# Kernel optimization log

Hardware: AMD Instinct MI355X
Metric: run time of the kernel (lower is better)

The kernel has to match this reference:

```python
import jax, jax.numpy as jnp
import numpy as np
import math

N, D, H, KV, DH, E, F_, CH = 2048, 1024, 16, 4, 64, 8, 2048, 64
VOCAB = 32000
EPS = 1e-6
THETA = 10000.0
DT = 0.1
BASE_SCALE = 10.0


def rmsnorm(x, w):
    var = jnp.mean(jnp.square(x), axis=-1, keepdims=True)
    return x * jax.lax.rsqrt(var + EPS) * w


def rope_tables(positions):
    inv_freq = THETA ** (-jnp.arange(0, DH, 2, dtype=jnp.float32) / DH)  # [DH/2]
    ang = positions.astype(jnp.float32)[:, None] * inv_freq              # [N, DH/2]
    return jnp.cos(ang), jnp.sin(ang)


def apply_rotary(x, cos, sin):
    # x: [N, heads, DH]; NeoX half-split rotation
    x1, x2 = jnp.split(x, 2, axis=-1)
    c, s = cos[:, None, :], sin[:, None, :]
    return jnp.concatenate([x1 * c - x2 * s, x2 * c + x1 * s], axis=-1)


def setup_inputs() -> dict:
    key = jax.random.key(0)
    ks = jax.random.split(key, 20)
    nrm = lambda k, shp, std: (jax.random.normal(k, shp) * std).astype(jnp.float32)
    inp = {
        'hidden': jax.random.normal(ks[0], (N, D), jnp.float32),
        'positions': jnp.arange(N, dtype=jnp.int32),
        'velocity': jax.random.normal(ks[1], (N, D), jnp.float32) * 0.1,
        'token_ids': jax.random.randint(ks[2], (N,), 0, VOCAB),
        'mu_prev': jax.random.normal(ks[3], (N, D), jnp.float32) * 0.1,
        'ln1_w': jnp.ones((D,), jnp.float32),
        'ln2_w': jnp.ones((D,), jnp.float32),
        'wq': nrm(ks[4], (D, H * DH), 0.02),
        'wk': nrm(ks[5], (D, KV * DH), 0.02),
        'wv': nrm(ks[6], (D, KV * DH), 0.02),
        'wo': nrm(ks[7], (H * DH, D), 0.02),
        'w_mu_q': nrm(ks[8], (D, H * DH), 0.01),
        'w_mu_k': nrm(ks[9], (D, KV * DH), 0.01),
        'w_mu_v': nrm(ks[10], (D, KV * DH), 0.01),
        'qnorm_w': jnp.ones((DH,), jnp.float32),
        'knorm_w': jnp.ones((DH,), jnp.float32),
        'dyn_mu': jnp.zeros((D,), jnp.float32),
        'dyn_mu_proj_w': nrm(ks[11], (D, D), 0.01),
        'ctrl_in_w': nrm(ks[12], (2 * D, CH), 0.02),
        'ctrl_in_b': jnp.zeros((CH,), jnp.float32),
        'ctrl_out_w': nrm(ks[13], (CH, 3 * D), 0.01),
        'ctrl_out_b': jnp.concatenate([jnp.full((D,), 2.2), jnp.full((D,), -2.2), jnp.zeros((D,))]).astype(jnp.float32),
        'mu_router_w': nrm(ks[14], (D, E), 0.01),
        'w_gate': nrm(ks[15], (E, D, F_), 0.02),
        'w_up': nrm(ks[16], (E, D, F_), 0.02),
        'w_down': nrm(ks[17], (E, F_, D), 0.02),
    }
    return inp


def reference(hidden, positions, velocity, token_ids, mu_prev,
              ln1_w, ln2_w, wq, wk, wv, wo, w_mu_q, w_mu_k, w_mu_v,
              qnorm_w, knorm_w, dyn_mu, dyn_mu_proj_w,
              ctrl_in_w, ctrl_in_b, ctrl_out_w, ctrl_out_b,
              mu_router_w, w_gate, w_up, w_down):
    residual = hidden
    h = rmsnorm(hidden, ln1_w)
    # --- mu-guided GQA attention ---
    q = (h @ wq + mu_prev @ w_mu_q).reshape(N, H, DH)
    k = (h @ wk + mu_prev @ w_mu_k).reshape(N, KV, DH)
    v = (h @ wv + mu_prev @ w_mu_v).reshape(N, KV, DH)
    q = rmsnorm(q, qnorm_w)
    k = rmsnorm(k, knorm_w)
    cos, sin = rope_tables(positions)
    q = apply_rotary(q, cos, sin)
    k = apply_rotary(k, cos, sin)
    groups = H // KV
    k = jnp.repeat(k, groups, axis=1)  # [N, H, DH]
    v = jnp.repeat(v, groups, axis=1)
    scale = 1.0 / math.sqrt(DH)
    scores = jnp.einsum('nhd,mhd->hnm', q, k) * scale
    attn = jax.nn.softmax(scores, axis=-1)
    o = jnp.einsum('hnm,mhd->nhd', attn, v).reshape(N, H * DH) @ wo
    # --- INL dynamics (PID) ---
    hv = jnp.concatenate([o, velocity], axis=-1)
    ctrl = jax.nn.silu(hv @ ctrl_in_w + ctrl_in_b)
    co = ctrl @ ctrl_out_w + ctrl_out_b
    alpha_raw, beta_raw, gate_raw = co[:, :D], co[:, D:2 * D], co[:, 2 * D:]
    alpha = jax.nn.sigmoid(alpha_raw)
    beta = jnp.minimum(jax.nn.softplus(beta_raw), 2.0)
    gate = jax.nn.sigmoid(gate_raw)
    mu_cur = dyn_mu + o @ dyn_mu_proj_w
    err = o - mu_cur
    v_next = jnp.clip(alpha * velocity - beta * err, -10.0, 10.0)
    h_next = o + DT * gate * v_next
    hidden = residual + h_next
    # --- mu-guided token-routed MoE MLP ---
    residual2 = hidden
    x = rmsnorm(hidden, ln2_w)
    base_ids = (token_ids % E).astype(jnp.int32)
    mu_logits = mu_cur @ mu_router_w                        # [N, E]
    combined = jax.nn.one_hot(base_ids, E) * BASE_SCALE + mu_logits
    expert_ids = jnp.argmax(combined, axis=-1)              # [N]
    g = jnp.einsum('nd,edf->enf', x, w_gate)                # [E, N, F]
    u = jnp.einsum('nd,edf->enf', x, w_up)
    mid = jax.nn.silu(g) * u
    y_all = jnp.einsum('enf,efd->end', mid, w_down)         # [E, N, D]
    sel = jax.nn.one_hot(expert_ids, E)                     # [N, E]
    y = jnp.einsum('ne,end->nd', sel, y_all)
    hidden = residual2 + y
    return (hidden, v_next, mu_cur)
```

## Files before the change

### kernel.cpp

```cpp
#include <hip/hip_runtime.h>
#include <hip/hip_bf16.h>
#include <math.h>

typedef __hip_bfloat16 bf16;
typedef __attribute__((ext_vector_type(8))) short short8;
typedef __attribute__((ext_vector_type(4))) float floatx4;

#define N_TOK 2048
#define DM    1024
#define NH    16
#define NKV   4
#define DH    64
#define NE    8
#define FF    2048
#define CH    64

__device__ __forceinline__ float b2f(bf16 x) { return __bfloat162float(x); }
__device__ __forceinline__ bf16  f2b(float x) { return __float2bfloat16(x); }
__device__ __forceinline__ short f2s(float x) { bf16 t = __float2bfloat16(x); return *(short*)&t; }

#define GLL16(g, l) __builtin_amdgcn_global_load_lds( \
    (const __attribute__((address_space(1))) void*)(g), \
    (__attribute__((address_space(3))) void*)(l), 16, 0, 0)

__device__ __forceinline__ float blockReduceSum256(float v) {
    __shared__ float tmp[4];
    #pragma unroll
    for (int m = 1; m < 64; m <<= 1) v += __shfl_xor(v, m, 64);
    if ((threadIdx.x & 63) == 0) tmp[threadIdx.x >> 6] = v;
    __syncthreads();
    float r = tmp[0] + tmp[1] + tmp[2] + tmp[3];
    __syncthreads();
    return r;
}

__global__ __launch_bounds__(256) void k_transpose(
    const float* __restrict__ src, long sstrideE, int sN,
    bf16* __restrict__ dst, long dstrideE, int ldk)
{
    __shared__ float tile[64][65];
    const float* s = src + (long)blockIdx.z * sstrideE;
    bf16* d = dst + (long)blockIdx.z * dstrideE;
    int n0 = blockIdx.x * 64, k0 = blockIdx.y * 64;
    int tid = threadIdx.x;
    int c = tid & 63, r4 = tid >> 6;
    #pragma unroll
    for (int i = 0; i < 16; i++) {
        int r = i * 4 + r4;
        tile[r][c] = s[(long)(k0 + r) * sN + n0 + c];
    }
    __syncthreads();
    int c2 = (tid & 31) * 2, rr = tid >> 5;
    #pragma unroll
    for (int i = 0; i < 8; i++) {
        int r = i * 8 + rr;
        short2 o;
        o.x = f2s(tile[c2][r]);
        o.y = f2s(tile[c2 + 1][r]);
        *(short2*)(d + (long)(n0 + r) * ldk + k0 + c2) = o;
    }
}

__global__ __launch_bounds__(256) void k_prep(
    const float* __restrict__ hidden, const float* __restrict__ ln1_w,
    const float* __restrict__ mu_prev, const float* __restrict__ velocity,
    bf16* __restrict__ catA, bf16* __restrict__ ctrlA)
{
    int n = blockIdx.x, tid = threadIdx.x;
    float ss = 0.f, vals[4];
    #pragma unroll
    for (int i = 0; i < 4; i++) {
        int c = tid + i * 256;
        vals[i] = hidden[(long)n * DM + c];
        ss += vals[i] * vals[i];
        catA[(long)n * 2048 + 1024 + c] = f2b(mu_prev[(long)n * DM + c]);
        ctrlA[(long)n * 2048 + 1024 + c] = f2b(velocity[(long)n * DM + c]);
    }
    float tot = blockReduceSum256(ss);
    float r = rsqrtf(tot / (float)DM + 1e-6f);
    #pragma unroll
    for (int i = 0; i < 4; i++) {
        int c = tid + i * 256;
        catA[(long)n * 2048 + c] = f2b(vals[i] * r * ln1_w[c]);
    }
}

#define GEMM_WRITE  1
#define GEMM_BIAS   2
#define GEMM_WRITEB 4
#define GEMM_DOWN   8

__global__ __launch_bounds__(256) void k_gemm(
    const bf16* __restrict__ A, int lda,
    const bf16* __restrict__ Bt, int ldb, long strideBe,
    float* __restrict__ C, int ldc,
    const float* __restrict__ bias,
    bf16* __restrict__ Cb, int ldcb,
    int K, int flags,
    int nsplit, long strideKc,
    const int* __restrict__ grp_off,
    const int* __restrict__ perm,
    float* __restrict__ outp)
{
    __shared__ __align__(16) short As[128 * 32];
    __shared__ __align__(16) short Bs[128 * 32];
    int tid = threadIdx.x;
    int e = blockIdx.z, kc = 0;
    if (nsplit > 1) { e = blockIdx.z / nsplit; kc = blockIdx.z % nsplit; }
    int rowBase, rowsValid;
    const bf16* Bp = Bt;
    if (grp_off) {
        int r0 = grp_off[e], r1 = grp_off[e + 1];
        int rt = blockIdx.y * 128;
        rowsValid = (r1 - r0) - rt;
        if (rowsValid <= 0) return;
        if (rowsValid > 128) rowsValid = 128;
        rowBase = r0 + rt;
        Bp = Bt + (long)e * strideBe;
    } else {
        rowBase = blockIdx.y * 128;
        rowsValid = 128;
    }
    int n0 = blockIdx.x * 128;
    int Kc = K / nsplit;
    int kbeg = kc * Kc, kend = kbeg + Kc;

    floatx4 acc[4][4];
    #pragma unroll
    for (int i = 0; i < 4; i++)
        #pragma unroll
        for (int j = 0; j < 4; j++) acc[i][j] = (floatx4){0.f, 0.f, 0.f, 0.f};

    int wave = tid >> 6, lane = tid & 63;
    int wm = (wave >> 1) * 64, wn = (wave & 1) * 64;
    int lrow = lane & 15, quad = lane >> 4;

    int c0 = wave * 2;
    int srow0 = c0 * 16 + (lane >> 2);
    int srow1 = (c0 + 1) * 16 + (lane >> 2);
    int skoff = (lane & 3) * 8;
    short* ldsA0 = As + c0 * 512;
    short* ldsA1 = As + (c0 + 1) * 512;
    short* ldsB0 = Bs + c0 * 512;
    short* ldsB1 = Bs + (c0 + 1) * 512;

    for (int k0 = kbeg; k0 < kend; k0 += 32) {
        if (srow0 < rowsValid) GLL16(A + (long)(rowBase + srow0) * lda + k0 + skoff, ldsA0);
        if (srow1 < rowsValid) GLL16(A + (long)(rowBase + srow1) * lda + k0 + skoff, ldsA1);
        GLL16(Bp + (long)(n0 + srow0) * ldb + k0 + skoff, ldsB0);
        GLL16(Bp + (long)(n0 + srow1) * ldb + k0 + skoff, ldsB1);
        __syncthreads();
        short8 af[4], bfr[4];
        #pragma unroll
        for (int mi = 0; mi < 4; mi++)
            af[mi] = *(const short8*)(&As[(wm + mi * 16 + lrow) * 32 + quad * 8]);
        #pragma unroll
        for (int ni = 0; ni < 4; ni++)
            bfr[ni] = *(const short8*)(&Bs[(wn + ni * 16 + lrow) * 32 + quad * 8]);
        #pragma unroll
        for (int mi = 0; mi < 4; mi++)
            #pragma unroll
            for (int ni = 0; ni < 4; ni++)
                acc[mi][ni] = __builtin_amdgcn_mfma_f32_16x16x32_bf16(
                    af[mi], bfr[ni], acc[mi][ni], 0, 0, 0);
        __syncthreads();
    }

    #pragma unroll
    for (int mi = 0; mi < 4; mi++) {
        #pragma unroll
        for (int ni = 0; ni < 4; ni++) {
            #pragma unroll
            for (int r = 0; r < 4; r++) {
                int rl = wm + mi * 16 + quad * 4 + r;
                if (rl >= rowsValid) continue;
                int grow = rowBase + rl;
                int gcol = n0 + wn + ni * 16 + lrow;
                float v = acc[mi][ni][r];
                if (nsplit > 1) {
                    C[kc * strideKc + (long)grow * ldc + gcol] = v;
                    continue;
                }
                if (flags & GEMM_BIAS) v += bias[gcol];
                if (flags & GEMM_DOWN) {
                    int tok = perm[grow];
                    float* o = &outp[(long)tok * ldc + gcol];
                    *o = *o + v;
                } else {
                    if (flags & GEMM_WRITE) C[(long)grow * ldc + gcol] = v;
                    if (flags & GEMM_WRITEB) Cb[(long)grow * ldcb + gcol] = f2b(v);
                }
            }
        }
    }
}

__global__ __launch_bounds__(256) void k_red_wo(const float* __restrict__ p,
                                                float* __restrict__ o_f,
                                                bf16* __restrict__ ctrlA) {
    int n = blockIdx.x, tid = threadIdx.x;
    #pragma unroll
    for (int i = 0; i < 4; i++) {
        int c = tid + i * 256;
        float v = p[(long)n * DM + c] + p[(long)N_TOK * DM + (long)n * DM + c];
        o_f[(long)n * DM + c] = v;
        ctrlA[(long)n * 2048 + c] = f2b(v);
    }
}

__global__ __launch_bounds__(256) void k_red_down(const float* __restrict__ p,
                                                  const int* __restrict__ perm,
                                                  float* __restrict__ out0) {
    int r = blockIdx.x, tid = threadIdx.x;
    int tok = perm[r];
    #pragma unroll
    for (int i = 0; i < 4; i++) {
        int c = tid + i * 256;
        long idx = (long)r * DM + c;
        float v = p[idx] + p[(long)N_TOK * DM + idx] +
                  p[(long)2 * N_TOK * DM + idx] + p[(long)3 * N_TOK * DM + idx];
        out0[(long)tok * DM + c] += v;
    }
}

__global__ __launch_bounds__(256) void k_ctrl_gemm(
    const bf16* __restrict__ A,
    const bf16* __restrict__ Bt,
    float* __restrict__ part)
{
    __shared__ __align__(16) short As[128 * 32];
    __shared__ __align__(16) short Bs[64 * 32];
    int tid = threadIdx.x;
    int rowBase = blockIdx.x * 128;
    int kbeg = blockIdx.y * 256;
    int wave = tid >> 6, lane = tid & 63;
    int wm = wave * 32, lrow = lane & 15, quad = lane >> 4;
    int srow = lane >> 2, skoff = (lane & 3) * 8;

    floatx4 acc[2][4];
    #pragma unroll
    for (int i = 0; i < 2; i++)
        #pragma unroll
        for (int j = 0; j < 4; j++) acc[i][j] = (floatx4){0.f, 0.f, 0.f, 0.f};

    short* ldsA0 = As + (wave * 2) * 512;
    short* ldsA1 = As + (wave * 2 + 1) * 512;
    short* ldsB  = Bs + wave * 512;

    for (int k0 = kbeg; k0 < kbeg + 256; k0 += 32) {
        GLL16(A + (long)(rowBase + wave * 32 + srow) * 2048 + k0 + skoff, ldsA0);
        GLL16(A + (long)(rowBase + wave * 32 + 16 + srow) * 2048 + k0 + skoff, ldsA1);
        GLL16(Bt + (long)(wave * 16 + srow) * 2048 + k0 + skoff, ldsB);
        __syncthreads();
        short8 af[2], bfr[4];
        af[0] = *(const short8*)(&As[(wm + lrow) * 32 + quad * 8]);
        af[1] = *(const short8*)(&As[(wm + 16 + lrow) * 32 + quad * 8]);
        #pragma unroll
        for (int ni = 0; ni < 4; ni++)
            bfr[ni] = *(const short8*)(&Bs[(ni * 16 + lrow) * 32 + quad * 8]);
        #pragma unroll
        for (int mi = 0; mi < 2; mi++)
            #pragma unroll
            for (int ni = 0; ni < 4; ni++)
                acc[mi][ni] = __builtin_amdgcn_mfma_f32_16x16x32_bf16(
                    af[mi], bfr[ni], acc[mi][ni], 0, 0, 0);
        __syncthreads();
    }
    #pragma unroll
    for (int mi = 0; mi < 2; mi++)
        #pragma unroll
        for (int ni = 0; ni < 4; ni++)
            #pragma unroll
            for (int r = 0; r < 4; r++) {
                int grow = rowBase + wm + mi * 16 + quad * 4 + r;
                part[((long)blockIdx.y * N_TOK + grow) * 64 + ni * 16 + lrow] = acc[mi][ni][r];
            }
}

__global__ __launch_bounds__(256) void k_silu_ctrl(const float* __restrict__ part,
                                                   const float* __restrict__ b,
                                                   bf16* __restrict__ out) {
    int i = blockIdx.x * 256 + threadIdx.x;
    float a = b[i & 63];
    #pragma unroll
    for (int kc = 0; kc < 8; kc++) a += part[(long)kc * (N_TOK * 64) + i];
    out[i] = f2b(a / (1.f + __expf(-a)));
}

__global__ __launch_bounds__(256) void k_qkv_post(
    const float* __restrict__ qkvp, const int* __restrict__ positions,
    const float* __restrict__ qnw, const float* __restrict__ knw,
    bf16* __restrict__ q, bf16* __restrict__ k, bf16* __restrict__ v)
{
    int n = blockIdx.x;
    int wave = threadIdx.x >> 6, lane = threadIdx.x & 63;
    float pos = (float)positions[n];
    int i = lane & 31;
    float invf = exp2f(-(float)(2 * i) * (13.287712379549449f / 64.f));
    float ang = pos * invf;
    float c = cosf(ang), s = sinf(ang);

    #pragma unroll
    for (int si = 0; si < 6; si++) {
        int slot = wave + si * 4;
        long base = (long)n * 1536 +
                    (slot < 16 ? slot * 64
                               : (slot < 20 ? 1024 + (slot - 16) * 64
                                            : 1280 + (slot - 20) * 64));
        float val = qkvp[base + lane] + qkvp[(long)N_TOK * 1536 + base + lane];
        if (slot < 20) {
            float ss = val * val;
            #pragma unroll
            for (int m = 1; m < 64; m <<= 1) ss += __shfl_xor(ss, m, 64);
            float r = rsqrtf(ss / 64.f + 1e-6f);
            float wn = (slot < 16 ? qnw[lane] : knw[lane]);
            float xn = val * r * wn;
            float partner = __shfl_xor(xn, 32, 64);
            float out = (lane < 32) ? (xn * c - partner * s) : (xn * c + partner * s);
            if (slot < 16) q[((long)n * NH + slot) * 64 + lane] = f2b(out);
            else           k[((long)n * NKV + (slot - 16)) * 64 + lane] = f2b(out);
        } else {
            v[((long)n * NKV + (slot - 20)) * 64 + lane] = f2b(val);
        }
    }
}

__global__ __launch_bounds__(256) void k_vt(const bf16* __restrict__ v,
                                            bf16* __restrict__ vt) {
    __shared__ short tile[64][65];
    int kv = blockIdx.z, n0 = blockIdx.x * 64;
    int tid = threadIdx.x;
    int c = tid & 63, r4 = tid >> 6;
    const short* vs = (const short*)v;
    #pragma unroll
    for (int i = 0; i < 16; i++) {
        int r = i * 4 + r4;
        tile[r][c] = vs[(long)(n0 + r) * 256 + kv * 64 + c];
    }
    __syncthreads();
    #pragma unroll
    for (int i = 0; i < 16; i++) {
        int d = i * 4 + r4;
        ((short*)vt)[(long)(kv * 64 + d) * 2048 + n0 + c] = tile[c][d];
    }
}

__global__ __launch_bounds__(256) void k_attn(
    const bf16* __restrict__ q, const bf16* __restrict__ k,
    const bf16* __restrict__ vt,
    float* __restrict__ opart, float2* __restrict__ ml)
{
    const int h = blockIdx.y;
    const int qbase = blockIdx.x * 64;
    const int z = blockIdx.z;
    const int kvh = h >> 2;
    __shared__ __align__(16) short Qs[64 * 72];
    __shared__ __align__(16) short Ks[64 * 72];
    __shared__ __align__(16) short Vt[64 * 72];
    __shared__ __align__(16) short Ps[4 * 16 * 72];
    int tid = threadIdx.x, wave = tid >> 6, lane = tid & 63;
    int lrow = lane & 15, quad = lane >> 4;

    #pragma unroll
    for (int i = 0; i < 2; i++) {
        int lin = tid + i * 256;
        int r = lin >> 3, dc = (lin & 7) << 3;
        short8 vq = *(const short8*)(q + ((long)(qbase + r) * NH + h) * 64 + dc);
        *(short8*)&Qs[r * 72 + dc] = vq;
    }
    float m_i[4], l_i[4];
    floatx4 oacc[4];
    #pragma unroll
    for (int r = 0; r < 4; r++) { m_i[r] = -1e30f; l_i[r] = 0.f; }
    #pragma unroll
    for (int di = 0; di < 4; di++) oacc[di] = (floatx4){0.f, 0.f, 0.f, 0.f};
    const float scale = 0.125f;
    __syncthreads();

    const int kt0 = z * (N_TOK / 2);
    for (int kt = kt0; kt < kt0 + N_TOK / 2; kt += 64) {
        #pragma unroll
        for (int i = 0; i < 2; i++) {
            int lin = tid + i * 256;
            int r = lin >> 3, dc = (lin & 7) << 3;
            short8 k8 = *(const short8*)(k + ((long)(kt + r) * NKV + kvh) * 64 + dc);
            *(short8*)&Ks[r * 72 + dc] = k8;
            short8 v8 = *(const short8*)(vt + (long)(kvh * 64 + r) * 2048 + kt + dc);
            *(short8*)&Vt[r * 72 + dc] = v8;
        }
        __syncthreads();

        short8 aq0 = *(const short8*)&Qs[(wave * 16 + lrow) * 72 + quad * 8];
        short8 aq1 = *(const short8*)&Qs[(wave * 16 + lrow) * 72 + 32 + quad * 8];
        floatx4 sv[4];
        #pragma unroll
        for (int kn = 0; kn < 4; kn++) {
            short8 b0 = *(const short8*)&Ks[(kn * 16 + lrow) * 72 + quad * 8];
            short8 b1 = *(const short8*)&Ks[(kn * 16 + lrow) * 72 + 32 + quad * 8];
            floatx4 t = (floatx4){0.f, 0.f, 0.f, 0.f};
            t = __builtin_amdgcn_mfma_f32_16x16x32_bf16(aq0, b0, t, 0, 0, 0);
            t = __builtin_amdgcn_mfma_f32_16x16x32_bf16(aq1, b1, t, 0, 0, 0);
            sv[kn] = t;
        }
        #pragma unroll
        for (int kn = 0; kn < 4; kn++)
            #pragma unroll
            for (int r = 0; r < 4; r++) sv[kn][r] *= scale;

        #pragma unroll
        for (int r = 0; r < 4; r++) {
            float mx = fmaxf(fmaxf(sv[0][r], sv[1][r]), fmaxf(sv[2][r], sv[3][r]));
            #pragma unroll
            for (int msk = 1; msk < 16; msk <<= 1) mx = fmaxf(mx, __shfl_xor(mx, msk, 64));
            float mnew = fmaxf(m_i[r], mx);
            float alpha = __expf(m_i[r] - mnew);
            m_i[r] = mnew;
            l_i[r] *= alpha;
            #pragma unroll
            for (int di = 0; di < 4; di++) oacc[di][r] *= alpha;
            float rowsum = 0.f;
            #pragma unroll
            for (int kn = 0; kn < 4; kn++) {
                float pp = __expf(sv[kn][r] - mnew);
                sv[kn][r] = pp;
                rowsum += pp;
            }
            #pragma unroll
            for (int msk = 1; msk < 16; msk <<= 1) rowsum += __shfl_xor(rowsum, msk, 64);
            l_i[r] += rowsum;
        }
        #pragma unroll
        for (int kn = 0; kn < 4; kn++)
            #pragma unroll
            for (int r = 0; r < 4; r++)
                Ps[(wave * 16 + quad * 4 + r) * 72 + kn * 16 + lrow] = f2s(sv[kn][r]);
        __syncthreads();

        short8 ap0 = *(const short8*)&Ps[(wave * 16 + lrow) * 72 + quad * 8];
        short8 ap1 = *(const short8*)&Ps[(wave * 16 + lrow) * 72 + 32 + quad * 8];
        #pragma unroll
        for (int di = 0; di < 4; di++) {
            short8 bv0 = *(const short8*)&Vt[(di * 16 + lrow) * 72 + quad * 8];
            short8 bv1 = *(const short8*)&Vt[(di * 16 + lrow) * 72 + 32 + quad * 8];
            oacc[di] = __builtin_amdgcn_mfma_f32_16x16x32_bf16(ap0, bv0, oacc[di], 0, 0, 0);
            oacc[di] = __builtin_amdgcn_mfma_f32_16x16x32_bf16(ap1, bv1, oacc[di], 0, 0, 0);
        }
        __syncthreads();
    }

    #pragma unroll
    for (int di = 0; di < 4; di++)
        #pragma unroll
        for (int r = 0; r < 4; r++) {
            int n = qbase + wave * 16 + quad * 4 + r;
            opart[((long)z * N_TOK + n) * DM + h * 64 + di * 16 + lrow] = oacc[di][r];
        }
    if (lrow == 0) {
        #pragma unroll
        for (int r = 0; r < 4; r++) {
            int n = qbase + wave * 16 + quad * 4 + r;
            ml[(long)(z * NH + h) * N_TOK + n] = make_float2(m_i[r], l_i[r]);
        }
    }
}

__global__ __launch_bounds__(256) void k_attn_merge(
    const float* __restrict__ opart, const float2* __restrict__ ml,
    bf16* __restrict__ attn_out)
{
    int n = blockIdx.x, tid = threadIdx.x;
    __shared__ float2 sml[2][NH];
    if (tid < 32) {
        int z = tid >> 4, hh = tid & 15;
        sml[z][hh] = ml[(long)(z * NH + hh) * N_TOK + n];
    }
    __syncthreads();
    #pragma unroll
    for (int i = 0; i < 4; i++) {
        int c = tid + i * 256;
        int h = c >> 6;
        float2 a = sml[0][h], b = sml[1][h];
        float M = fmaxf(a.x, b.x);
        float w0 = __expf(a.x - M), w1 = __expf(b.x - M);
        float num = w0 * opart[(long)n * DM + c] +
                    w1 * opart[((long)N_TOK + n) * DM + c];
        float den = w0 * a.y + w1 * b.y;
        attn_out[(long)n * DM + c] = f2b(num / den);
    }
}

__global__ __launch_bounds__(256) void k_ode(
    const float* __restrict__ co, const float* __restrict__ o_f,
    const float* __restrict__ velocity, const float* __restrict__ mup,
    const float* __restrict__ dyn_mu, const float* __restrict__ hidden_in,
    const float* __restrict__ mu_router_w, const int* __restrict__ token_ids,
    const float* __restrict__ ln2_w,
    float* __restrict__ out0, float* __restrict__ out_vnext,
    float* __restrict__ out_mu, bf16* __restrict__ x_bf,
    int* __restrict__ expert_id, int* __restrict__ counts)
{
    int n = blockIdx.x, tid = threadIdx.x;
    __shared__ float mu_s[DM];
    __shared__ float red2[32][8];

    #pragma unroll
    for (int i = 0; i < 4; i++) {
        int c = tid + i * 256;
        mu_s[c] = mup[(long)n * DM + c] + mup[(long)N_TOK * DM + (long)n * DM + c]
                + dyn_mu[c];
    }
    __syncthreads();

    {
        int e = tid & 7, kc = tid >> 3;
        float a = 0.f;
        #pragma unroll
        for (int kk = 0; kk < 32; kk++) {
            int k = kc * 32 + kk;
            a += mu_s[k] * mu_router_w[k * NE + e];
        }
        red2[kc][e] = a;
    }
    __syncthreads();
    if (tid == 0) {
        int bid = token_ids[n] & (NE - 1);
        float best = -1e30f; int bi = 0;
        for (int e = 0; e < NE; e++) {
            float lg = (e == bid ? 10.f : 0.f);
            for (int j = 0; j < 32; j++) lg += red2[j][e];
            if (lg > best) { best = lg; bi = e; }
        }
        expert_id[n] = bi;
        atomicAdd(&counts[bi], 1);
    }

    float ssq = 0.f;
    float h1v[4];
    #pragma unroll
    for (int i = 0; i < 4; i++) {
        int c = tid + i * 256;
        float coa = co[(long)n * 3072 + c];
        float cob = co[(long)n * 3072 + DM + c];
        float cog = co[(long)n * 3072 + 2 * DM + c];
        float alpha = 1.f / (1.f + __expf(-coa));
        float sp = (cob > 20.f) ? cob : log1pf(__expf(cob));
        float beta = fminf(sp, 2.0f);
        float gate = 1.f / (1.f + __expf(-cog));
        float ov = o_f[(long)n * DM + c];
        float vv = velocity[(long)n * DM + c];
        float err = ov - mu_s[c];
        float vn = fminf(fmaxf(alpha * vv - beta * err, -10.f), 10.f);
        float hn = ov + 0.1f * gate * vn;
        float h1 = hidden_in[(long)n * DM + c] + hn;
        h1v[i] = h1;
        ssq += h1 * h1;
        out_vnext[(long)n * DM + c] = vn;
        out_mu[(long)n * DM + c] = mu_s[c];
        out0[(long)n * DM + c] = h1;
    }
    float tot = blockReduceSum256(ssq);
    float rstd = rsqrtf(tot / (float)DM + 1e-6f);
    #pragma unroll
    for (int i = 0; i < 4; i++) {
        int c = tid + i * 256;
        x_bf[(long)n * DM + c] = f2b(h1v[i] * rstd * ln2_w[c]);
    }
}

__global__ void k_zero8(int* counts, int* fill) {
    if (threadIdx.x < NE) { counts[threadIdx.x] = 0; fill[threadIdx.x] = 0; }
}
__global__ void k_offsets(const int* counts, int* off) {
    if (threadIdx.x == 0) {
        int a = 0;
        for (int e = 0; e < NE; e++) { off[e] = a; a += counts[e]; }
        off[NE] = a;
    }
}
__global__ void k_scatter(const int* expert_id, const int* off, int* fill, int* perm) {
    int n = blockIdx.x * 256 + threadIdx.x;
    if (n < N_TOK) {
        int e = expert_id[n];
        int p = off[e] + atomicAdd(&fill[e], 1);
        perm[p] = n;
    }
}
__global__ __launch_bounds__(256) void k_gather(const int* __restrict__ perm,
                                                const bf16* __restrict__ x,
                                                bf16* __restrict__ xg) {
    int r = blockIdx.x;
    int tok = perm[r];
    ((int2*)(xg + (long)r * DM))[threadIdx.x] =
        ((const int2*)(x + (long)tok * DM))[threadIdx.x];
}
__global__ __launch_bounds__(256) void k_silumul(const bf16* __restrict__ gu,
                                                 bf16* __restrict__ mid) {
    long i = (long)blockIdx.x * 256 + threadIdx.x;
    long r = i >> 11, c = i & 2047;
    float g = b2f(gu[r * 4096 + c]);
    float u = b2f(gu[r * 4096 + 2048 + c]);
    mid[i] = f2b(g / (1.f + __expf(-g)) * u);
}

extern "C" void kernel_launch(void* const* d_in, const int* in_sizes, int n_in,
                              void* d_out, int out_size, void* d_ws, size_t ws_size,
                              hipStream_t stream) {
    (void)in_sizes; (void)n_in; (void)out_size; (void)ws_size;
    const float* hidden     = (const float*)d_in[0];
    const int*   positions  = (const int*)d_in[1];
    const float* velocity   = (const float*)d_in[2];
    const int*   token_ids  = (const int*)d_in[3];
    const float* mu_prev    = (const float*)d_in[4];
    const float* ln1_w      = (const float*)d_in[5];
    const float* ln2_w      = (const float*)d_in[6];
    const float* wq         = (const float*)d_in[7];
    const float* wk         = (const float*)d_in[8];
    const float* wv         = (const float*)d_in[9];
    const float* wo         = (const float*)d_in[10];
    const float* w_mu_q     = (const float*)d_in[11];
    const float* w_mu_k     = (const float*)d_in[12];
    const float* w_mu_v     = (const float*)d_in[13];
    const float* qnorm_w    = (const float*)d_in[14];
    const float* knorm_w    = (const float*)d_in[15];
    const float* dyn_mu     = (const float*)d_in[16];
    const float* dyn_proj   = (const float*)d_in[17];
    const float* ctrl_in_w  = (const float*)d_in[18];
    const float* ctrl_in_b  = (const float*)d_in[19];
    const float* ctrl_out_w = (const float*)d_in[20];
    const float* ctrl_out_b = (const float*)d_in[21];
    const float* mu_router  = (const float*)d_in[22];
    const float* w_gate     = (const float*)d_in[23];
    const float* w_up       = (const float*)d_in[24];
    const float* w_down     = (const float*)d_in[25];

    float* out0 = (float*)d_out;
    float* out1 = out0 + (long)N_TOK * DM;
    float* out2 = out1 + (long)N_TOK * DM;

    char* p = (char*)d_ws;
    auto alloc = [&](size_t bytes) -> void* {
        void* r = (void*)p;
        p += (bytes + 255) & ~(size_t)255;
        return r;
    };
    bf16* WqkvT   = (bf16*)alloc((long)1536 * 2048 * 2);
    bf16* woT     = (bf16*)alloc((long)1024 * 1024 * 2);
    bf16* dynT    = (bf16*)alloc((long)1024 * 1024 * 2);
    bf16* ctrlinT = (bf16*)alloc((long)64 * 2048 * 2);
    bf16* ctrloutT= (bf16*)alloc((long)3072 * 64 * 2);
    bf16* gupT    = (bf16*)alloc((long)NE * 4096 * 1024 * 2);
    bf16* downT   = (bf16*)alloc((long)NE * 1024 * 2048 * 2);
    bf16*  catA   = (bf16*)alloc((long)N_TOK * 2048 * 2);
    bf16*  ctrlA  = (bf16*)alloc((long)N_TOK * 2048 * 2);
    float* xbuf   = (float*)alloc((long)N_TOK * 1536 * 4);
    bf16*  q_bf   = (bf16*)alloc((long)N_TOK * NH * DH * 2);
    bf16*  k_bf   = (bf16*)alloc((long)N_TOK * NKV * DH * 2);
    bf16*  v_bf   = (bf16*)alloc((long)N_TOK * NKV * DH * 2);
    bf16*  vt_bf  = (bf16*)alloc((long)NKV * DH * N_TOK * 2);
    float* o_f    = (float*)alloc((long)N_TOK * DM * 4);
    float* coGu   = (float*)alloc((long)N_TOK * 3072 * 4);
    float* splitb = (float*)alloc((long)4 * N_TOK * DM * 4);
    bf16*  ctrlbf = (bf16*)alloc((long)N_TOK * CH * 2);
    int*   expert_id = (int*)alloc(N_TOK * 4);
    int*   perm      = (int*)alloc(N_TOK * 4);
    int*   counts    = (int*)alloc(64 * 4);
    int*   fill      = (int*)alloc(64 * 4);
    int*   offs      = (int*)alloc(64 * 4);

    bf16*  attn_bf = catA;
    bf16*  x_bf    = (bf16*)xbuf;
    bf16*  xg_bf   = (bf16*)xbuf + (long)N_TOK * DM;
    float* cpart   = (float*)((bf16*)xbuf + (long)2 * N_TOK * DM);
    float* opart   = coGu;
    float2* ml     = (float2*)(coGu + (long)2 * N_TOK * DM);
    float* co_f    = coGu;
    bf16*  gu_bf   = (bf16*)coGu;
    bf16*  mid_bf  = (bf16*)o_f;

    dim3 blk(256);
    k_zero8<<<1, 64, 0, stream>>>(counts, fill);

    k_transpose<<<dim3(16,16,1), blk, 0, stream>>>(wq, 0, 1024, WqkvT, 0, 2048);
    k_transpose<<<dim3(4,16,1),  blk, 0, stream>>>(wk, 0, 256,  WqkvT + (long)1024*2048, 0, 2048);
    k_transpose<<<dim3(4,16,1),  blk, 0, stream>>>(wv, 0, 256,  WqkvT + (long)1280*2048, 0, 2048);
    k_transpose<<<dim3(16,16,1), blk, 0, stream>>>(w_mu_q, 0, 1024, WqkvT + 1024, 0, 2048);
    k_transpose<<<dim3(4,16,1),  blk, 0, stream>>>(w_mu_k, 0, 256,  WqkvT + (long)1024*2048 + 1024, 0, 2048);
    k_transpose<<<dim3(4,16,1),  blk, 0, stream>>>(w_mu_v, 0, 256,  WqkvT + (long)1280*2048 + 1024, 0, 2048);
    k_transpose<<<dim3(16,16,1), blk, 0, stream>>>(wo, 0, 1024, woT, 0, 1024);
    k_transpose<<<dim3(16,16,1), blk, 0, stream>>>(dyn_proj, 0, 1024, dynT, 0, 1024);
    k_transpose<<<dim3(1,32,1),  blk, 0, stream>>>(ctrl_in_w, 0, 64, ctrlinT, 0, 2048);
    k_transpose<<<dim3(48,1,1),  blk, 0, stream>>>(ctrl_out_w, 0, 3072, ctrloutT, 0, 64);
    k_transpose<<<dim3(32,16,NE), blk, 0, stream>>>(w_gate, (long)1024*2048, 2048,
        gupT, (long)4096*1024, 1024);
    k_transpose<<<dim3(32,16,NE), blk, 0, stream>>>(w_up, (long)1024*2048, 2048,
        gupT + (long)2048*1024, (long)4096*1024, 1024);
    k_transpose<<<dim3(16,32,NE), blk, 0, stream>>>(w_down, (long)2048*1024, 1024,
        downT, (long)1024*2048, 2048);

    k_prep<<<N_TOK, blk, 0, stream>>>(hidden, ln1_w, mu_prev, velocity, catA, ctrlA);

    k_gemm<<<dim3(12,16,2), blk, 0, stream>>>(catA, 2048, WqkvT, 2048, 0,
        splitb, 1536, nullptr, nullptr, 0, 2048, 0, 2, (long)N_TOK * 1536,
        nullptr, nullptr, nullptr);

    k_qkv_post<<<N_TOK, blk, 0, stream>>>(splitb, positions, qnorm_w, knorm_w, q_bf, k_bf, v_bf);
    k_vt<<<dim3(32,1,NKV), blk, 0, stream>>>(v_bf, vt_bf);
    k_attn<<<dim3(32,16,2), blk, 0, stream>>>(q_bf, k_bf, vt_bf, opart, ml);
    k_attn_merge<<<N_TOK, blk, 0, stream>>>(opart, ml, attn_bf);

    k_gemm<<<dim3(8,16,2), blk, 0, stream>>>(attn_bf, 1024, woT, 1024, 0,
        splitb, 1024, nullptr, nullptr, 0, 1024, 0, 2, (long)N_TOK * DM,
        nullptr, nullptr, nullptr);
    k_red_wo<<<N_TOK, blk, 0, stream>>>(splitb, o_f, ctrlA);

    k_gemm<<<dim3(8,16,2), blk, 0, stream>>>(ctrlA, 2048, dynT, 1024, 0,
        splitb, 1024, nullptr, nullptr, 0, 1024, 0, 2, (long)N_TOK * DM,
        nullptr, nullptr, nullptr);

    k_ctrl_gemm<<<dim3(16,8,1), blk, 0, stream>>>(ctrlA, ctrlinT, cpart);
    k_silu_ctrl<<<(N_TOK * CH) / 256, blk, 0, stream>>>(cpart, ctrl_in_b, ctrlbf);
    k_gemm<<<dim3(24,16,1), blk, 0, stream>>>(ctrlbf, 64, ctrloutT, 64, 0,
        co_f, 3072, ctrl_out_b, nullptr, 0, 64, GEMM_WRITE | GEMM_BIAS, 1, 0,
        nullptr, nullptr, nullptr);

    k_ode<<<N_TOK, blk, 0, stream>>>(co_f, o_f, velocity, splitb, dyn_mu, hidden,
        mu_router, token_ids, ln2_w, out0, out1, out2, x_bf, expert_id, counts);

    k_offsets<<<1, 64, 0, stream>>>(counts, offs);
    k_scatter<<<NE, blk, 0, stream>>>(expert_id, offs, fill, perm);
    k_gather<<<N_TOK, blk, 0, stream>>>(perm, x_bf, xg_bf);

    k_gemm<<<dim3(32,16,NE), blk, 0, stream>>>(xg_bf, 1024, gupT, 1024, (long)4096*1024,
        nullptr, 0, nullptr, gu_bf, 4096, 1024, GEMM_WRITEB, 1, 0,
        offs, nullptr, nullptr);
    k_silumul<<<(N_TOK * FF) / 256, blk, 0, stream>>>(gu_bf, mid_bf);
    k_gemm<<<dim3(8,16,NE*4), blk, 0, stream>>>(mid_bf, 2048, downT, 2048, (long)1024*2048,
        splitb, 1024, nullptr, nullptr, 0, 2048, 0, 4, (long)N_TOK * DM,
        offs, nullptr, nullptr);
    k_red_down<<<N_TOK, blk, 0, stream>>>(splitb, perm, out0);
}
```

Before: 648.0 us.

## Batch weight transposes, fuse MoE routing kernels, and rework attention with 4-way split

All thirteen weight transposes, plus the counter zeroing, now run as one table-driven launch with vectorized loads and stores. The offsets, scatter and gather kernels become one kernel that computes prefix offsets inline, and the grouped GEMM derives its row offsets from the counts. Attention moves to a 4-way KV split with a swizzled LDS layout and register-prefetched K/V tiles. It also folds the softmax scale and log2e into Q so exp2 can be used, skips the rescale when the running max grows by less than a threshold, and computes row sums with an MFMA against a ones vector. Buffers are reassigned to fit the larger partial outputs. This cuts launch overhead, LDS bank conflicts and attention latency, at the cost of more merge work and some bf16 precision in the row sums.

```diff
diff --git a/kernel.cpp b/kernel.cpp
--- a/kernel.cpp
+++ b/kernel.cpp
@@ -14,10 +14,13 @@
 #define NE    8
 #define FF    2048
 #define CH    64
+#define QSCL  0.18033688011112042f
 
 __device__ __forceinline__ float b2f(bf16 x) { return __bfloat162float(x); }
 __device__ __forceinline__ bf16  f2b(float x) { return __float2bfloat16(x); }
 __device__ __forceinline__ short f2s(float x) { bf16 t = __float2bfloat16(x); return *(short*)&t; }
+
+#define MFMA16(a, b, c) __builtin_amdgcn_mfma_f32_16x16x32_bf16(a, b, c, 0, 0, 0)
 
 #define GLL16(g, l) __builtin_amdgcn_global_load_lds( \
     (const __attribute__((address_space(1))) void*)(g), \
@@ -34,30 +37,51 @@
     return r;
 }
 
-__global__ __launch_bounds__(256) void k_transpose(
-    const float* __restrict__ src, long sstrideE, int sN,
-    bf16* __restrict__ dst, long dstrideE, int ldk)
-{
-    __shared__ float tile[64][65];
-    const float* s = src + (long)blockIdx.z * sstrideE;
-    bf16* d = dst + (long)blockIdx.z * dstrideE;
-    int n0 = blockIdx.x * 64, k0 = blockIdx.y * 64;
+struct TEnt {
+    const float* src; bf16* dst;
+    long sstride, dstride;
+    int sN, ldk, tN, tilesPer, start;
+};
+struct TTab { TEnt t[13]; };
+
+__global__ __launch_bounds__(256) void k_transpose_all(TTab tab, int* counts, int* fill) {
+    if (blockIdx.x == 0 && threadIdx.x < NE) {
+        counts[threadIdx.x] = 0;
+        fill[threadIdx.x] = 0;
+    }
+    int b = blockIdx.x;
+    int wi = 0;
+    #pragma unroll
+    for (int i = 1; i < 13; i++) if (b >= tab.t[i].start) wi = i;
+    const TEnt& w = tab.t[wi];
+    int local = b - w.start;
+    int e = local / w.tilesPer; local -= e * w.tilesPer;
+    int kt = local / w.tN, nt = local - kt * w.tN;
+    const float* s = w.src + (long)e * w.sstride;
+    bf16* d = w.dst + (long)e * w.dstride;
+    int n0 = nt * 64, k0 = kt * 64;
+
+    __shared__ float t[64][65];
     int tid = threadIdx.x;
-    int c = tid & 63, r4 = tid >> 6;
-    #pragma unroll
-    for (int i = 0; i < 16; i++) {
-        int r = i * 4 + r4;
-        tile[r][c] = s[(long)(k0 + r) * sN + n0 + c];
+    int c4 = (tid & 15) * 4, r0 = tid >> 4;
+    #pragma unroll
+    for (int i = 0; i < 4; i++) {
+        int row = r0 + i * 16;
+        float4 v = *(const float4*)(s + (long)(k0 + row) * w.sN + n0 + c4);
+        t[c4 + 0][row] = v.x;
+        t[c4 + 1][row] = v.y;
+        t[c4 + 2][row] = v.z;
+        t[c4 + 3][row] = v.w;
     }
     __syncthreads();
-    int c2 = (tid & 31) * 2, rr = tid >> 5;
-    #pragma unroll
-    for (int i = 0; i < 8; i++) {
-        int r = i * 8 + rr;
-        short2 o;
-        o.x = f2s(tile[c2][r]);
-        o.y = f2s(tile[c2 + 1][r]);
-        *(short2*)(d + (long)(n0 + r) * ldk + k0 + c2) = o;
+    int k8 = (tid & 7) * 8, nr = tid >> 3;
+    #pragma unroll
+    for (int i = 0; i < 2; i++) {
+        int nn = nr + i * 32;
+        short8 o;
+        #pragma unroll
+        for (int j = 0; j < 8; j++) o[j] = f2s(t[nn][k8 + j]);
+        *(short8*)(d + (long)(n0 + nn) * w.ldk + k0 + k8) = o;
     }
 }
 
@@ -98,7 +122,7 @@
     bf16* __restrict__ Cb, int ldcb,
     int K, int flags,
     int nsplit, long strideKc,
-    const int* __restrict__ grp_off,
+    const int* __restrict__ grp_cnt,
     const int* __restrict__ perm,
     float* __restrict__ outp)
 {
@@ -109,8 +133,11 @@
     if (nsplit > 1) { e = blockIdx.z / nsplit; kc = blockIdx.z % nsplit; }
     int rowBase, rowsValid;
     const bf16* Bp = Bt;
-    if (grp_off) {
-        int r0 = grp_off[e], r1 = grp_off[e + 1];
+    if (grp_cnt) {
+        int r0 = 0;
+        #pragma unroll
+        for (int i = 0; i < NE; i++) r0 += (i < e) ? grp_cnt[i] : 0;
+        int r1 = r0 + grp_cnt[e];
         int rt = blockIdx.y * 128;
         rowsValid = (r1 - r0) - rt;
         if (rowsValid <= 0) return;
@@ -161,8 +188,7 @@
         for (int mi = 0; mi < 4; mi++)
             #pragma unroll
             for (int ni = 0; ni < 4; ni++)
-                acc[mi][ni] = __builtin_amdgcn_mfma_f32_16x16x32_bf16(
-                    af[mi], bfr[ni], acc[mi][ni], 0, 0, 0);
+                acc[mi][ni] = MFMA16(af[mi], bfr[ni], acc[mi][ni]);
         __syncthreads();
     }
 
@@ -262,8 +288,7 @@
         for (int mi = 0; mi < 2; mi++)
             #pragma unroll
             for (int ni = 0; ni < 4; ni++)
-                acc[mi][ni] = __builtin_amdgcn_mfma_f32_16x16x32_bf16(
-                    af[mi], bfr[ni], acc[mi][ni], 0, 0, 0);
+                acc[mi][ni] = MFMA16(af[mi], bfr[ni], acc[mi][ni]);
         __syncthreads();
     }
     #pragma unroll
@@ -317,7 +342,7 @@
             float xn = val * r * wn;
             float partner = __shfl_xor(xn, 32, 64);
             float out = (lane < 32) ? (xn * c - partner * s) : (xn * c + partner * s);
-            if (slot < 16) q[((long)n * NH + slot) * 64 + lane] = f2b(out);
+            if (slot < 16) q[((long)n * NH + slot) * 64 + lane] = f2b(out * QSCL);
             else           k[((long)n * NKV + (slot - 16)) * 64 + lane] = f2b(out);
         } else {
             v[((long)n * NKV + (slot - 20)) * 64 + lane] = f2b(val);
@@ -343,6 +368,12 @@
         int d = i * 4 + r4;
         ((short*)vt)[(long)(kv * 64 + d) * 2048 + n0 + c] = tile[c][d];
     }
+}
+
+__device__ __forceinline__ int lds_idx(int row, int col_sh) {
+    int byteoff = col_sh * 2;
+    byteoff ^= (row & 7) << 4;
+    return row * 64 + (byteoff >> 1);
 }
 
 __global__ __launch_bounds__(256) void k_attn(
@@ -354,98 +385,127 @@
     const int qbase = blockIdx.x * 64;
     const int z = blockIdx.z;
     const int kvh = h >> 2;
-    __shared__ __align__(16) short Qs[64 * 72];
-    __shared__ __align__(16) short Ks[64 * 72];
-    __shared__ __align__(16) short Vt[64 * 72];
-    __shared__ __align__(16) short Ps[4 * 16 * 72];
+    __shared__ __align__(16) short Ks[64 * 64];
+    __shared__ __align__(16) short Vt[64 * 64];
+    __shared__ __align__(16) short Ps[64 * 64];
     int tid = threadIdx.x, wave = tid >> 6, lane = tid & 63;
     int lrow = lane & 15, quad = lane >> 4;
 
-    #pragma unroll
-    for (int i = 0; i < 2; i++) {
-        int lin = tid + i * 256;
-        int r = lin >> 3, dc = (lin & 7) << 3;
-        short8 vq = *(const short8*)(q + ((long)(qbase + r) * NH + h) * 64 + dc);
-        *(short8*)&Qs[r * 72 + dc] = vq;
-    }
-    float m_i[4], l_i[4];
+    const bf16* qp = q + ((long)(qbase + wave * 16 + lrow) * NH + h) * 64;
+    short8 aq0 = *(const short8*)(qp + quad * 8);
+    short8 aq1 = *(const short8*)(qp + 32 + quad * 8);
+
+    short8 bones;
+    #pragma unroll
+    for (int j = 0; j < 8; j++) bones[j] = (short)0x3F80;
+
+    const int lin0 = tid, lin1 = tid + 256;
+    const int sr0 = lin0 >> 3, sc0 = (lin0 & 7) * 8;
+    const int sr1 = lin1 >> 3, sc1 = (lin1 & 7) * 8;
+    const int wi0 = lds_idx(sr0, sc0), wi1 = lds_idx(sr1, sc1);
+
+    const int kt0 = z * (N_TOK / 4);
+    const bf16* kg0 = k + ((long)(kt0 + sr0) * NKV + kvh) * 64 + sc0;
+    const bf16* kg1 = k + ((long)(kt0 + sr1) * NKV + kvh) * 64 + sc1;
+    const bf16* vg0 = vt + (long)(kvh * 64 + sr0) * 2048 + kt0 + sc0;
+    const bf16* vg1 = vt + (long)(kvh * 64 + sr1) * 2048 + kt0 + sc1;
+
+    *(short8*)&Ks[wi0] = *(const short8*)kg0;
+    *(short8*)&Ks[wi1] = *(const short8*)kg1;
+    *(short8*)&Vt[wi0] = *(const short8*)vg0;
+    *(short8*)&Vt[wi1] = *(const short8*)vg1;
+
+    float m_i[4];
+    floatx4 lacc = (floatx4){0.f, 0.f, 0.f, 0.f};
     floatx4 oacc[4];
     #pragma unroll
-    for (int r = 0; r < 4; r++) { m_i[r] = -1e30f; l_i[r] = 0.f; }
+    for (int r = 0; r < 4; r++) m_i[r] = -1e30f;
     #pragma unroll
     for (int di = 0; di < 4; di++) oacc[di] = (floatx4){0.f, 0.f, 0.f, 0.f};
-    const float scale = 0.125f;
     __syncthreads();
 
-    const int kt0 = z * (N_TOK / 2);
-    for (int kt = kt0; kt < kt0 + N_TOK / 2; kt += 64) {
-        #pragma unroll
-        for (int i = 0; i < 2; i++) {
-            int lin = tid + i * 256;
-            int r = lin >> 3, dc = (lin & 7) << 3;
-            short8 k8 = *(const short8*)(k + ((long)(kt + r) * NKV + kvh) * 64 + dc);
-            *(short8*)&Ks[r * 72 + dc] = k8;
-            short8 v8 = *(const short8*)(vt + (long)(kvh * 64 + r) * 2048 + kt + dc);
-            *(short8*)&Vt[r * 72 + dc] = v8;
-        }
-        __syncthreads();
-
-        short8 aq0 = *(const short8*)&Qs[(wave * 16 + lrow) * 72 + quad * 8];
-        short8 aq1 = *(const short8*)&Qs[(wave * 16 + lrow) * 72 + 32 + quad * 8];
+    const int NT = (N_TOK / 4) / 64;
+    for (int t = 0; t < NT; t++) {
+        bool pf = (t + 1 < NT);
+        short8 nk0, nk1, nv0, nv1;
+        if (pf) {
+            long ko = (long)(t + 1) * (64 * NKV * 64);
+            int  vo = (t + 1) * 64;
+            nk0 = *(const short8*)(kg0 + ko);
+            nk1 = *(const short8*)(kg1 + ko);
+            nv0 = *(const short8*)(vg0 + vo);
+            nv1 = *(const short8*)(vg1 + vo);
+        }
+
         floatx4 sv[4];
+        __builtin_amdgcn_s_setprio(1);
         #pragma unroll
         for (int kn = 0; kn < 4; kn++) {
-            short8 b0 = *(const short8*)&Ks[(kn * 16 + lrow) * 72 + quad * 8];
-            short8 b1 = *(const short8*)&Ks[(kn * 16 + lrow) * 72 + 32 + quad * 8];
-            floatx4 t = (floatx4){0.f, 0.f, 0.f, 0.f};
-            t = __builtin_amdgcn_mfma_f32_16x16x32_bf16(aq0, b0, t, 0, 0, 0);
-            t = __builtin_amdgcn_mfma_f32_16x16x32_bf16(aq1, b1, t, 0, 0, 0);
-            sv[kn] = t;
-        }
-        #pragma unroll
-        for (int kn = 0; kn < 4; kn++)
+            short8 b0 = *(const short8*)&Ks[lds_idx(kn * 16 + lrow, quad * 8)];
+            short8 b1 = *(const short8*)&Ks[lds_idx(kn * 16 + lrow, 32 + quad * 8)];
+            floatx4 tt = (floatx4){0.f, 0.f, 0.f, 0.f};
+            tt = MFMA16(aq0, b0, tt);
+            tt = MFMA16(aq1, b1, tt);
+            sv[kn] = tt;
+        }
+        __builtin_amdgcn_s_setprio(0);
+
+        float mx[4];
+        #pragma unroll
+        for (int r = 0; r < 4; r++) {
+            float m0 = fmaxf(fmaxf(sv[0][r], sv[1][r]), fmaxf(sv[2][r], sv[3][r]));
             #pragma unroll
-            for (int r = 0; r < 4; r++) sv[kn][r] *= scale;
-
-        #pragma unroll
-        for (int r = 0; r < 4; r++) {
-            float mx = fmaxf(fmaxf(sv[0][r], sv[1][r]), fmaxf(sv[2][r], sv[3][r]));
+            for (int msk = 1; msk < 16; msk <<= 1) m0 = fmaxf(m0, __shfl_xor(m0, msk, 64));
+            mx[r] = m0;
+        }
+        int ok = (mx[0] <= m_i[0] + 8.f) & (mx[1] <= m_i[1] + 8.f) &
+                 (mx[2] <= m_i[2] + 8.f) & (mx[3] <= m_i[3] + 8.f);
+        if (!__all(ok)) {
             #pragma unroll
-            for (int msk = 1; msk < 16; msk <<= 1) mx = fmaxf(mx, __shfl_xor(mx, msk, 64));
-            float mnew = fmaxf(m_i[r], mx);
-            float alpha = __expf(m_i[r] - mnew);
-            m_i[r] = mnew;
-            l_i[r] *= alpha;
-            #pragma unroll
-            for (int di = 0; di < 4; di++) oacc[di][r] *= alpha;
-            float rowsum = 0.f;
-            #pragma unroll
-            for (int kn = 0; kn < 4; kn++) {
-                float pp = __expf(sv[kn][r] - mnew);
-                sv[kn][r] = pp;
-                rowsum += pp;
+            for (int r = 0; r < 4; r++) {
+                float mn = fmaxf(m_i[r], mx[r]);
+                float al = exp2f(m_i[r] - mn);
+                m_i[r] = mn;
+                lacc[r] *= al;
+                #pragma unroll
+                for (int di = 0; di < 4; di++) oacc[di][r] *= al;
             }
-            #pragma unroll
-            for (int msk = 1; msk < 16; msk <<= 1) rowsum += __shfl_xor(rowsum, msk, 64);
-            l_i[r] += rowsum;
         }
         #pragma unroll
         for (int kn = 0; kn < 4; kn++)
             #pragma unroll
             for (int r = 0; r < 4; r++)
-                Ps[(wave * 16 + quad * 4 + r) * 72 + kn * 16 + lrow] = f2s(sv[kn][r]);
+                sv[kn][r] = exp2f(sv[kn][r] - m_i[r]);
+
+        #pragma unroll
+        for (int kn = 0; kn < 4; kn++)
+            #pragma unroll
+            for (int r = 0; r < 4; r++)
+                Ps[lds_idx(wave * 16 + quad * 4 + r, kn * 16 + lrow)] = f2s(sv[kn][r]);
         __syncthreads();
 
-        short8 ap0 = *(const short8*)&Ps[(wave * 16 + lrow) * 72 + quad * 8];
-        short8 ap1 = *(const short8*)&Ps[(wave * 16 + lrow) * 72 + 32 + quad * 8];
+        short8 ap0 = *(const short8*)&Ps[lds_idx(wave * 16 + lrow, quad * 8)];
+        short8 ap1 = *(const short8*)&Ps[lds_idx(wave * 16 + lrow, 32 + quad * 8)];
+        __builtin_amdgcn_s_setprio(1);
+        lacc = MFMA16(ap0, bones, lacc);
+        lacc = MFMA16(ap1, bones, lacc);
         #pragma unroll
         for (int di = 0; di < 4; di++) {
-            short8 bv0 = *(const short8*)&Vt[(di * 16 + lrow) * 72 + quad * 8];
-            short8 bv1 = *(const short8*)&Vt[(di * 16 + lrow) * 72 + 32 + quad * 8];
-            oacc[di] = __builtin_amdgcn_mfma_f32_16x16x32_bf16(ap0, bv0, oacc[di], 0, 0, 0);
-            oacc[di] = __builtin_amdgcn_mfma_f32_16x16x32_bf16(ap1, bv1, oacc[di], 0, 0, 0);
-        }
+            short8 bv0 = *(const short8*)&Vt[lds_idx(di * 16 + lrow, quad * 8)];
+            short8 bv1 = *(const short8*)&Vt[lds_idx(di * 16 + lrow, 32 + quad * 8)];
+            oacc[di] = MFMA16(ap0, bv0, oacc[di]);
+            oacc[di] = MFMA16(ap1, bv1, oacc[di]);
+        }
+        __builtin_amdgcn_s_setprio(0);
         __syncthreads();
+
+        if (pf) {
+            *(short8*)&Ks[wi0] = nk0;
+            *(short8*)&Ks[wi1] = nk1;
+            *(short8*)&Vt[wi0] = nv0;
+            *(short8*)&Vt[wi1] = nv1;
+            __syncthreads();
+        }
     }
 
     #pragma unroll
@@ -459,7 +519,7 @@
         #pragma unroll
         for (int r = 0; r < 4; r++) {
             int n = qbase + wave * 16 + quad * 4 + r;
-            ml[(long)(z * NH + h) * N_TOK + n] = make_float2(m_i[r], l_i[r]);
+            ml[(long)(z * NH + h) * N_TOK + n] = make_float2(m_i[r], lacc[r]);
         }
     }
 }
@@ -469,22 +529,25 @@
     bf16* __restrict__ attn_out)
 {
     int n = blockIdx.x, tid = threadIdx.x;
-    __shared__ float2 sml[2][NH];
-    if (tid < 32) {
-        int z = tid >> 4, hh = tid & 15;
-        sml[z][hh] = ml[(long)(z * NH + hh) * N_TOK + n];
+    __shared__ float2 sml[4][NH];
+    if (tid < 64) {
+        int zz = tid >> 4, hh = tid & 15;
+        sml[zz][hh] = ml[(long)(zz * NH + hh) * N_TOK + n];
     }
     __syncthreads();
     #pragma unroll
     for (int i = 0; i < 4; i++) {
         int c = tid + i * 256;
         int h = c >> 6;
-        float2 a = sml[0][h], b = sml[1][h];
-        float M = fmaxf(a.x, b.x);
-        float w0 = __expf(a.x - M), w1 = __expf(b.x - M);
-        float num = w0 * opart[(long)n * DM + c] +
-                    w1 * opart[((long)N_TOK + n) * DM + c];
-        float den = w0 * a.y + w1 * b.y;
+        float M = fmaxf(fmaxf(sml[0][h].x, sml[1][h].x),
+                        fmaxf(sml[2][h].x, sml[3][h].x));
+        float num = 0.f, den = 0.f;
+        #pragma unroll
+        for (int zz = 0; zz < 4; zz++) {
+            float w = exp2f(sml[zz][h].x - M);
+            num += w * opart[((long)zz * N_TOK + n) * DM + c];
+            den += w * sml[zz][h].y;
+        }
         attn_out[(long)n * DM + c] = f2b(num / den);
     }
 }
@@ -567,32 +630,29 @@
     }
 }
 
-__global__ void k_zero8(int* counts, int* fill) {
-    if (threadIdx.x < NE) { counts[threadIdx.x] = 0; fill[threadIdx.x] = 0; }
-}
-__global__ void k_offsets(const int* counts, int* off) {
-    if (threadIdx.x == 0) {
-        int a = 0;
-        for (int e = 0; e < NE; e++) { off[e] = a; a += counts[e]; }
-        off[NE] = a;
-    }
-}
-__global__ void k_scatter(const int* expert_id, const int* off, int* fill, int* perm) {
-    int n = blockIdx.x * 256 + threadIdx.x;
-    if (n < N_TOK) {
-        int e = expert_id[n];
-        int p = off[e] + atomicAdd(&fill[e], 1);
+__global__ __launch_bounds__(256) void k_scatter_gather(
+    const int* __restrict__ expert_id, const int* __restrict__ counts,
+    int* __restrict__ fill, int* __restrict__ perm,
+    const bf16* __restrict__ x, bf16* __restrict__ xg)
+{
+    int n = blockIdx.x * 4 + (threadIdx.x >> 6);
+    int lane = threadIdx.x & 63;
+    int e = expert_id[n];
+    int p = 0;
+    if (lane == 0) {
+        int off = 0;
+        #pragma unroll
+        for (int i = 0; i < NE; i++) off += (i < e) ? counts[i] : 0;
+        p = off + atomicAdd(&fill[e], 1);
         perm[p] = n;
     }
-}
-__global__ __launch_bounds__(256) void k_gather(const int* __restrict__ perm,
-                                                const bf16* __restrict__ x,
-                                                bf16* __restrict__ xg) {
-    int r = blockIdx.x;
-    int tok = perm[r];
-    ((int2*)(xg + (long)r * DM))[threadIdx.x] =
-        ((const int2*)(x + (long)tok * DM))[threadIdx.x];
-}
+    p = __shfl(p, 0, 64);
+    const int4* s = (const int4*)(x + (long)n * DM);
+    int4* d = (int4*)(xg + (long)p * DM);
+    d[lane] = s[lane];
+    d[lane + 64] = s[lane + 64];
+}
+
 __global__ __launch_bounds__(256) void k_silumul(const bf16* __restrict__ gu,
                                                  bf16* __restrict__ mid) {
     long i = (long)blockIdx.x * 256 + threadIdx.x;
@@ -665,37 +725,43 @@
     int*   perm      = (int*)alloc(N_TOK * 4);
     int*   counts    = (int*)alloc(64 * 4);
     int*   fill      = (int*)alloc(64 * 4);
-    int*   offs      = (int*)alloc(64 * 4);
 
     bf16*  attn_bf = catA;
     bf16*  x_bf    = (bf16*)xbuf;
     bf16*  xg_bf   = (bf16*)xbuf + (long)N_TOK * DM;
     float* cpart   = (float*)((bf16*)xbuf + (long)2 * N_TOK * DM);
-    float* opart   = coGu;
-    float2* ml     = (float2*)(coGu + (long)2 * N_TOK * DM);
+    float* opart   = splitb;
+    float2* ml     = (float2*)coGu;
     float* co_f    = coGu;
     bf16*  gu_bf   = (bf16*)coGu;
     bf16*  mid_bf  = (bf16*)o_f;
 
     dim3 blk(256);
-    k_zero8<<<1, 64, 0, stream>>>(counts, fill);
-
-    k_transpose<<<dim3(16,16,1), blk, 0, stream>>>(wq, 0, 1024, WqkvT, 0, 2048);
-    k_transpose<<<dim3(4,16,1),  blk, 0, stream>>>(wk, 0, 256,  WqkvT + (long)1024*2048, 0, 2048);
-    k_transpose<<<dim3(4,16,1),  blk, 0, stream>>>(wv, 0, 256,  WqkvT + (long)1280*2048, 0, 2048);
-    k_transpose<<<dim3(16,16,1), blk, 0, stream>>>(w_mu_q, 0, 1024, WqkvT + 1024, 0, 2048);
-    k_transpose<<<dim3(4,16,1),  blk, 0, stream>>>(w_mu_k, 0, 256,  WqkvT + (long)1024*2048 + 1024, 0, 2048);
-    k_transpose<<<dim3(4,16,1),  blk, 0, stream>>>(w_mu_v, 0, 256,  WqkvT + (long)1280*2048 + 1024, 0, 2048);
-    k_transpose<<<dim3(16,16,1), blk, 0, stream>>>(wo, 0, 1024, woT, 0, 1024);
-    k_transpose<<<dim3(16,16,1), blk, 0, stream>>>(dyn_proj, 0, 1024, dynT, 0, 1024);
-    k_transpose<<<dim3(1,32,1),  blk, 0, stream>>>(ctrl_in_w, 0, 64, ctrlinT, 0, 2048);
-    k_transpose<<<dim3(48,1,1),  blk, 0, stream>>>(ctrl_out_w, 0, 3072, ctrloutT, 0, 64);
-    k_transpose<<<dim3(32,16,NE), blk, 0, stream>>>(w_gate, (long)1024*2048, 2048,
-        gupT, (long)4096*1024, 1024);
-    k_transpose<<<dim3(32,16,NE), blk, 0, stream>>>(w_up, (long)1024*2048, 2048,
-        gupT + (long)2048*1024, (long)4096*1024, 1024);
-    k_transpose<<<dim3(16,32,NE), blk, 0, stream>>>(w_down, (long)2048*1024, 1024,
-        downT, (long)1024*2048, 2048);
+
+    TTab tt; int st = 0;
+    auto ent = [&](int i, const float* s, bf16* d, long ss, long ds,
+                   int sN, int ldk, int tN, int tK, int nE) {
+        tt.t[i].src = s; tt.t[i].dst = d;
+        tt.t[i].sstride = ss; tt.t[i].dstride = ds;
+        tt.t[i].sN = sN; tt.t[i].ldk = ldk;
+        tt.t[i].tN = tN; tt.t[i].tilesPer = tN * tK;
+        tt.t[i].start = st;
+        st += tN * tK * nE;
+    };
+    ent(0,  wq,         WqkvT,                          0, 0, 1024, 2048, 16, 16, 1);
+    ent(1,  wk,         WqkvT + (long)1024 * 2048,      0, 0, 256,  2048,  4, 16, 1);
+    ent(2,  wv,         WqkvT + (long)1280 * 2048,      0, 0, 256,  2048,  4, 16, 1);
+    ent(3,  w_mu_q,     WqkvT + 1024,                   0, 0, 1024, 2048, 16, 16, 1);
+    ent(4,  w_mu_k,     WqkvT + (long)1024 * 2048 + 1024, 0, 0, 256, 2048, 4, 16, 1);
+    ent(5,  w_mu_v,     WqkvT + (long)1280 * 2048 + 1024, 0, 0, 256, 2048, 4, 16, 1);
+    ent(6,  wo,         woT,                            0, 0, 1024, 1024, 16, 16, 1);
+    ent(7,  dyn_proj,   dynT,                           0, 0, 1024, 1024, 16, 16, 1);
+    ent(8,  ctrl_in_w,  ctrlinT,                        0, 0, 64,   2048,  1, 32, 1);
+    ent(9,  ctrl_out_w, ctrloutT,                       0, 0, 3072, 64,   48,  1, 1);
+    ent(10, w_gate,     gupT,                  (long)1024 * 2048, (long)4096 * 1024, 2048, 1024, 32, 16, 8);
+    ent(11, w_up,       gupT + (long)2048 * 1024, (long)1024 * 2048, (long)4096 * 1024, 2048, 1024, 32, 16, 8);
+    ent(12, w_down,     downT,                 (long)2048 * 1024, (long)1024 * 2048, 1024, 2048, 16, 32, 8);
+    k_transpose_all<<<st, blk, 0, stream>>>(tt, counts, fill);
 
     k_prep<<<N_TOK, blk, 0, stream>>>(hidden, ln1_w, mu_prev, velocity, catA, ctrlA);
 
@@ -705,7 +771,7 @@
 
     k_qkv_post<<<N_TOK, blk, 0, stream>>>(splitb, positions, qnorm_w, knorm_w, q_bf, k_bf, v_bf);
     k_vt<<<dim3(32,1,NKV), blk, 0, stream>>>(v_bf, vt_bf);
-    k_attn<<<dim3(32,16,2), blk, 0, stream>>>(q_bf, k_bf, vt_bf, opart, ml);
+    k_attn<<<dim3(32,16,4), blk, 0, stream>>>(q_bf, k_bf, vt_bf, opart, ml);
     k_attn_merge<<<N_TOK, blk, 0, stream>>>(opart, ml, attn_bf);
 
     k_gemm<<<dim3(8,16,2), blk, 0, stream>>>(attn_bf, 1024, woT, 1024, 0,
@@ -726,16 +792,15 @@
     k_ode<<<N_TOK, blk, 0, stream>>>(co_f, o_f, velocity, splitb, dyn_mu, hidden,
         mu_router, token_ids, ln2_w, out0, out1, out2, x_bf, expert_id, counts);
 
-    k_offsets<<<1, 64, 0, stream>>>(counts, offs);
-    k_scatter<<<NE, blk, 0, stream>>>(expert_id, offs, fill, perm);
-    k_gather<<<N_TOK, blk, 0, stream>>>(perm, x_bf, xg_bf);
+    k_scatter_gather<<<N_TOK / 4, blk, 0, stream>>>(expert_id, counts, fill, perm,
+        x_bf, xg_bf);
 
     k_gemm<<<dim3(32,16,NE), blk, 0, stream>>>(xg_bf, 1024, gupT, 1024, (long)4096*1024,
         nullptr, 0, nullptr, gu_bf, 4096, 1024, GEMM_WRITEB, 1, 0,
-        offs, nullptr, nullptr);
+        counts, nullptr, nullptr);
     k_silumul<<<(N_TOK * FF) / 256, blk, 0, stream>>>(gu_bf, mid_bf);
     k_gemm<<<dim3(8,16,NE*4), blk, 0, stream>>>(mid_bf, 2048, downT, 2048, (long)1024*2048,
         splitb, 1024, nullptr, nullptr, 0, 2048, 0, 4, (long)N_TOK * DM,
-        offs, nullptr, nullptr);
+        counts, nullptr, nullptr);
     k_red_down<<<N_TOK, blk, 0, stream>>>(splitb, perm, out0);
 }
```

Result: faster. 627.3 us (-3.2%).
